# Performance work log

Hardware: AMD Instinct MI355X
Metric: run time of the kernel (lower is better)

## Reference

```python
import jax, jax.numpy as jnp
import numpy as np

N = 20000        # nodes
E = 320000       # edges (avg degree 16)
F_IN = 128       # node_features
F2 = 64          # second_features (per-head out dim, LSTM hidden)
H = 8            # heads
D1 = H * F2      # 512, concat output of GATConv / LSTM input
NEG_SLOPE = 0.2  # GATConv default leaky_relu slope


def _gat_conv(x, src, dst, W, att_src, att_dst, bias):
    """PyG GATConv (concat=True, self-loops added, eval-mode dropout)."""
    n = x.shape[0]
    h = (x @ W).reshape(n, H, -1)                      # [N,H,F]
    a_s = (h * att_src).sum(-1)                        # [N,H]
    a_d = (h * att_dst).sum(-1)                        # [N,H]
    e = jax.nn.leaky_relu(a_s[src] + a_d[dst], NEG_SLOPE)   # [E',H]
    m = jax.ops.segment_max(e, dst, num_segments=n)    # [N,H]
    m = jnp.where(jnp.isfinite(m), m, 0.0)
    ex = jnp.exp(e - m[dst])
    denom = jax.ops.segment_sum(ex, dst, num_segments=n)
    alpha = ex / (denom[dst] + 1e-16)                  # [E',H]
    msg = h[src] * alpha[:, :, None]                   # [E',H,F]
    out = jax.ops.segment_sum(msg, dst, num_segments=n)  # [N,H,F]
    return out.reshape(n, -1) + bias                   # [N,H*F]


def _lstm_step(x, W_ih, W_hh, b_ih, b_hh):
    """Single-timestep PyTorch LSTM with zero initial (h0, c0). x: [N,D1]."""
    h0 = jnp.zeros((x.shape[0], F2), x.dtype)
    gates = x @ W_ih.T + b_ih + h0 @ W_hh.T + b_hh     # [N,4*F2]
    i, f, g, o = jnp.split(gates, 4, axis=-1)
    c = jax.nn.sigmoid(f) * 0.0 + jax.nn.sigmoid(i) * jnp.tanh(g)
    h = jax.nn.sigmoid(o) * jnp.tanh(c)
    return h, (h, c)


def setup_inputs() -> dict:
    key = jax.random.key(0)
    ks = jax.random.split(key, 16)

    def glorot(k, shape, fan_in):
        return jax.random.normal(k, shape, jnp.float32) * (1.0 / np.sqrt(fan_in))

    return {
        "x": jax.random.normal(ks[0], (N, F_IN), jnp.float32),
        "edge_index": jax.random.randint(ks[1], (2, E), 0, N, jnp.int32),
        "edge_weight": jax.random.uniform(ks[2], (E,), jnp.float32),
        # GATConv 1: F_IN -> H*F2
        "W1": glorot(ks[3], (F_IN, H * F2), F_IN),
        "att_src1": glorot(ks[4], (H, F2), F2),
        "att_dst1": glorot(ks[5], (H, F2), F2),
        "bias1": jnp.zeros((H * F2,), jnp.float32),
        # LSTM: input D1 -> hidden F2
        "W_ih": glorot(ks[6], (4 * F2, D1), D1),
        "W_hh": glorot(ks[7], (4 * F2, F2), F2),
        "b_ih": jnp.zeros((4 * F2,), jnp.float32),
        "b_hh": jnp.zeros((4 * F2,), jnp.float32),
        # GATConv 2: F2 -> H*F2
        "W2": glorot(ks[8], (F2, H * F2), F2),
        "att_src2": glorot(ks[9], (H, F2), F2),
        "att_dst2": glorot(ks[10], (H, F2), F2),
        "bias2": jnp.zeros((H * F2,), jnp.float32),
    }


def reference(x, edge_index, edge_weight, W1, att_src1, att_dst1, bias1,
              W_ih, W_hh, b_ih, b_hh, W2, att_src2, att_dst2, bias2):
    # edge_weight is accepted but unused, matching the original forward.
    loops = jnp.arange(N, dtype=edge_index.dtype)
    src = jnp.concatenate([edge_index[0], loops])      # add self-loops (PyG default)
    dst = jnp.concatenate([edge_index[1], loops])

    h = _gat_conv(x, src, dst, W1, att_src1, att_dst1, bias1)   # [N,512]
    h, hidden2 = _lstm_step(h, W_ih, W_hh, b_ih, b_hh)          # [N,64]
    h = jax.nn.relu(h)
    h = _gat_conv(h, src, dst, W2, att_src2, att_dst2, bias2)   # [N,512]
    return jax.nn.softmax(h, axis=1)
```

## Files before the change

### kernel.cpp

```cpp
#include <hip/hip_runtime.h>
#include <math.h>
#include <stdint.h>


__global__ void count_kernel(const int* __restrict__ dst, int* __restrict__ deg, int E) {
  int i = blockIdx.x * 256 + threadIdx.x;
  if (i < E) atomicAdd(&deg[dst[i]], 1);
}

__global__ void scan_kernel(const int* __restrict__ deg, int* __restrict__ rowptr, int n) {
  __shared__ int buf[1024];
  const int tid = threadIdx.x;
  const int i0 = tid * 20;
  int v[20];
  int tsum = 0;
#pragma unroll
  for (int k = 0; k < 20; ++k) {
    int i = i0 + k;
    v[k] = (i < n) ? (deg[i] + 1) : 0;
    tsum += v[k];
  }
  int incl = tsum;
  buf[tid] = incl;
  __syncthreads();
  for (int s = 1; s < 1024; s <<= 1) {
    int t = (tid >= (unsigned)s) ? buf[tid - s] : 0;
    __syncthreads();
    incl += t;
    buf[tid] = incl;
    __syncthreads();
  }
  int excl = incl - tsum;
#pragma unroll
  for (int k = 0; k < 20; ++k) {
    int i = i0 + k;
    if (i < n) rowptr[i] = excl;
    excl += v[k];
  }
  if (tid == 1023) rowptr[n] = incl;
}

__global__ void scatter_kernel(const int* __restrict__ src, const int* __restrict__ dst,
                               const int* __restrict__ rowptr, int* __restrict__ wp,
                               int* __restrict__ col, int E, int n) {
  int i = blockIdx.x * 256 + threadIdx.x;
  if (i < E) {
    int d = dst[i];
    int p = rowptr[d] + atomicAdd(&wp[d], 1);
    col[p] = src[i];
  } else if (i < E + n) {
    int d = i - E;
    int p = rowptr[d] + atomicAdd(&wp[d], 1);
    col[p] = d;
  }
}


__device__ __forceinline__ uint16_t bf16r(float x) {
  uint32_t u = __float_as_uint(x);
  return (uint16_t)((u + 0x7FFFu + ((u >> 16) & 1u)) >> 16);
}
__device__ __forceinline__ void bfsplit(float x, uint16_t& h, uint16_t& l) {
  h = bf16r(x);
  float hf = __uint_as_float((uint32_t)h << 16);
  l = bf16r(x - hf);
}
__device__ __forceinline__ void store4split(uint16_t* oh, uint16_t* ol, float4 v) {
  ushort4 h, l;
  bfsplit(v.x, h.x, l.x); bfsplit(v.y, h.y, l.y);
  bfsplit(v.z, h.z, l.z); bfsplit(v.w, h.w, l.w);
  *reinterpret_cast<ushort4*>(oh) = h;
  *reinterpret_cast<ushort4*>(ol) = l;
}

__device__ __forceinline__ void gload16(const uint16_t* g, uint16_t* l) {
  __builtin_amdgcn_global_load_lds(
      (const __attribute__((address_space(1))) uint32_t*)g,
      (__attribute__((address_space(3))) uint32_t*)l, 16, 0, 0);
}

using bf16x8 = __attribute__((ext_vector_type(8))) short;
using f32x4  = __attribute__((ext_vector_type(4))) float;


template <bool SPLIT_OUT>
__global__ __launch_bounds__(256) void gemm_mfma(
    const uint16_t* __restrict__ Ah, const uint16_t* __restrict__ Al,
    const uint16_t* __restrict__ Bh, const uint16_t* __restrict__ Bl,
    float* __restrict__ C, uint16_t* __restrict__ Ch, uint16_t* __restrict__ Cl,
    const float* __restrict__ bias,
    int M, int K, int lda, int aZ, int bZ, int ldc, int cZ, int biasZ) {
  constexpr int BM = 64, BN = 64, BK = 64;
  constexpr int PL = BM * BK;
  __shared__ __align__(16) uint16_t sAh[2 * PL], sAl[2 * PL];
  __shared__ __align__(16) uint16_t sBh[2 * PL], sBl[2 * PL];
  const int z = blockIdx.z;
  Ah += (size_t)z * aZ; Al += (size_t)z * aZ;
  Bh += (size_t)z * bZ; Bl += (size_t)z * bZ;
  const int tid = threadIdx.x;
  const int wid = tid >> 6, lane = tid & 63;
  int L = blockIdx.x + gridDim.x * blockIdx.y;
  int nwg = gridDim.x * gridDim.y;
  int q = nwg >> 3, r = nwg & 7;
  int xcd = L & 7, gix = L >> 3;
  int base = (xcd < r) ? xcd * (q + 1) : r * (q + 1) + (xcd - r) * q;
  int w = base + gix;
  const int bm = (w / gridDim.x) * BM;
  const int bn = (w % gridDim.x) * BN;
  const int fr = lane & 15;
  const int kg = lane >> 4;
  const int mbase = wid * 16;
  f32x4 acc[4] = {};

  auto stage = [&](int sb, int k0) {
#pragma unroll
    for (int j = 0; j < 2; ++j) {
      int idx = (wid * 2 + j) * 64 + lane;
      int row = idx >> 3, c = idx & 7;
      int rg = min(bm + row, M - 1);
      size_t goA = (size_t)rg * lda + k0 + ((c ^ (row & 7)) << 3);
      uint16_t* ldst = sAh + sb * PL + (wid * 2 + j) * 512;
      gload16(Ah + goA, ldst);
      gload16(Al + goA, sAl + sb * PL + (wid * 2 + j) * 512);
      size_t goB = (size_t)(bn + row) * K + k0 + ((c ^ (row & 7)) << 3);
      gload16(Bh + goB, sBh + sb * PL + (wid * 2 + j) * 512);
      gload16(Bl + goB, sBl + sb * PL + (wid * 2 + j) * 512);
    }
  };

  stage(0, 0);
  __syncthreads();
  int buf = 0;
  for (int k0 = 0; k0 < K; k0 += BK) {
    const bool more = (k0 + BK) < K;
    if (more) stage(buf ^ 1, k0 + BK);
    const char* pAh = (const char*)sAh + buf * (PL * 2);
    const char* pAl = (const char*)sAl + buf * (PL * 2);
    const char* pBh = (const char*)sBh + buf * (PL * 2);
    const char* pBl = (const char*)sBl + buf * (PL * 2);
#pragma unroll
    for (int ks = 0; ks < 2; ++ks) {
      const int kc = ks * 4 + kg;
      bf16x8 ah, al, bh[4], bl[4];
      {
        int m = mbase + fr;
        int off = m * 128 + ((kc ^ (m & 7)) << 4);
        ah = *reinterpret_cast<const bf16x8*>(pAh + off);
        al = *reinterpret_cast<const bf16x8*>(pAl + off);
      }
#pragma unroll
      for (int j = 0; j < 4; ++j) {
        int n = j * 16 + fr;
        int off = n * 128 + ((kc ^ (n & 7)) << 4);
        bh[j] = *reinterpret_cast<const bf16x8*>(pBh + off);
        bl[j] = *reinterpret_cast<const bf16x8*>(pBl + off);
      }
#pragma unroll
      for (int j = 0; j < 4; ++j) {
        acc[j] = __builtin_amdgcn_mfma_f32_16x16x32_bf16(ah, bh[j], acc[j], 0, 0, 0);
        acc[j] = __builtin_amdgcn_mfma_f32_16x16x32_bf16(al, bh[j], acc[j], 0, 0, 0);
        acc[j] = __builtin_amdgcn_mfma_f32_16x16x32_bf16(ah, bl[j], acc[j], 0, 0, 0);
      }
    }
    if (more) {
      __syncthreads();
      buf ^= 1;
    }
  }
  float bz[4];
#pragma unroll
  for (int j = 0; j < 4; ++j)
    bz[j] = bias ? bias[(size_t)z * biasZ + bn + j * 16 + fr] : 0.f;
  if (SPLIT_OUT) {
    Ch += (size_t)z * cZ;
    Cl += (size_t)z * cZ;
  } else {
    C += (size_t)z * cZ;
  }
  {
    int mr = bm + mbase + kg * 4;
#pragma unroll
    for (int rr = 0; rr < 4; ++rr) {
      int m = mr + rr;
      if (m < M) {
#pragma unroll
        for (int j = 0; j < 4; ++j) {
          float v = acc[j][rr] + bz[j];
          size_t o = (size_t)m * ldc + bn + j * 16 + fr;
          if (SPLIT_OUT) {
            uint16_t h, l;
            bfsplit(v, h, l);
            Ch[o] = h; Cl[o] = l;
          } else {
            C[o] = v;
          }
        }
      }
    }
  }
}


__global__ void prep_all_kernel(const float* __restrict__ W_ih, const float* __restrict__ b_ih,
                                const float* __restrict__ b_hh, const float* __restrict__ W1,
                                const float* __restrict__ as1, const float* __restrict__ ad1,
                                const float* __restrict__ W2, const float* __restrict__ as2,
                                const float* __restrict__ ad2,
                                int* __restrict__ degwp,
                                uint16_t* __restrict__ Wtbh, uint16_t* __restrict__ Wtbl,
                                uint16_t* __restrict__ Bt1h, uint16_t* __restrict__ Bt1l,
                                uint16_t* __restrict__ Bt2h, uint16_t* __restrict__ Bt2l,
                                float* __restrict__ bsum, float* __restrict__ watt1,
                                float* __restrict__ watt2, int n2) {
  int idx = blockIdx.x * 256 + threadIdx.x;
  if (idx < n2) {
    degwp[idx] = 0;
    return;
  }
  int t = idx - n2;
  if (t < 98304) {
    int jp = t >> 9, k = t & 511;
    int j = (jp < 64) ? jp : jp + 64;
    uint16_t h, l;
    bfsplit(W_ih[(size_t)j * 512 + k], h, l);
    Wtbh[t] = h; Wtbl[t] = l;
    return;
  }
  t -= 98304;
  if (t < 65536) {
    int n = t >> 7, k = t & 127;
    uint16_t h, l;
    bfsplit(W1[(size_t)k * 512 + n], h, l);
    Bt1h[t] = h; Bt1l[t] = l;
    return;
  }
  t -= 65536;
  if (t < 32768) {
    int n = t >> 6, k = t & 63;
    uint16_t h, l;
    bfsplit(W2[(size_t)k * 512 + n], h, l);
    Bt2h[t] = h; Bt2l[t] = l;
    return;
  }
  t -= 32768;
  if (t < 192) {
    int j = (t < 64) ? t : t + 64;
    bsum[t] = b_ih[j] + b_hh[j];
    return;
  }
  t -= 192;
  if (t < 2048) {
    int f = t >> 4, c = t & 15;
    int k = c & 7;
    const float* att = ((c < 8) ? as1 : ad1) + k * 64;
    const float* w = W1 + (size_t)f * 512 + k * 64;
    float s = 0.f;
#pragma unroll
    for (int j = 0; j < 64; ++j) s = fmaf(w[j], att[j], s);
    watt1[t] = s;
    return;
  }
  t -= 2048;
  if (t < 1024) {
    int f = t >> 4, c = t & 15;
    int k = c & 7;
    const float* att = ((c < 8) ? as2 : ad2) + k * 64;
    const float* w = W2 + (size_t)f * 512 + k * 64;
    float s = 0.f;
#pragma unroll
    for (int j = 0; j < 64; ++j) s = fmaf(w[j], att[j], s);
    watt2[t] = s;
  }
}


template <int F>
__global__ __launch_bounds__(256) void attcoef_kernel(
    const float* __restrict__ feat, const float* __restrict__ watt,
    float* __restrict__ a_s, float* __restrict__ a_d, int n) {
  __shared__ float rows[16 * F];
  __shared__ float wbuf[F * 16];
  const int n0 = blockIdx.x * 16;
  const int tid = threadIdx.x;
  if (n0 + 16 <= n) {
    const float4* g = reinterpret_cast<const float4*>(feat + (size_t)n0 * F);
    float4* l = reinterpret_cast<float4*>(rows);
    for (int i = tid; i < 16 * F / 4; i += 256) l[i] = g[i];
  } else {
    for (int i = tid; i < 16 * F; i += 256) {
      int r = i / F;
      rows[i] = (n0 + r < n) ? feat[(size_t)(n0 + r) * F + (i - r * F)] : 0.f;
    }
  }
  {
    const float4* g = reinterpret_cast<const float4*>(watt);
    float4* l = reinterpret_cast<float4*>(wbuf);
    for (int i = tid; i < F * 16 / 4; i += 256) l[i] = g[i];
  }
  __syncthreads();
  const int local = tid >> 4, c = tid & 15;
  float s = 0.f;
#pragma unroll 8
  for (int f = 0; f < F; ++f) s = fmaf(rows[local * F + f], wbuf[f * 16 + c], s);
  const int node = n0 + local;
  if (node < n) {
    if (c < 8) a_s[(size_t)node * 8 + c] = s;
    else       a_d[(size_t)node * 8 + (c - 8)] = s;
  }
}


template <int F>
__global__ __launch_bounds__(256) void gat_aggregate_wave(
    const float* __restrict__ feat, const float* __restrict__ a_s,
    const float* __restrict__ a_d, const int* __restrict__ rowptr,
    const int* __restrict__ col, uint16_t* __restrict__ aggH,
    uint16_t* __restrict__ aggL, int n) {
  constexpr int FL = F / 4;
  constexpr int HPW = (F == 128) ? 4 : 2;
  __shared__ float s_ex[4][8][8];
  __shared__ int s_cols[4][8];
  const int wid = threadIdx.x >> 6;
  const int lane = threadIdx.x & 63;
  const int node = blockIdx.x * 4 + wid;
  if (node >= n) return;
  const int start = rowptr[node];
  const int deg = rowptr[node + 1] - start;
  const int j = lane >> 3;
  const int h = lane & 7;
  const int f4 = lane & (FL - 1);
  const int hbase = (lane / FL) * HPW;
  const float adh = a_d[(size_t)node * 8 + h];
  float dpart = 0.f;
  float4 acc[HPW];
#pragma unroll
  for (int q = 0; q < HPW; ++q) acc[q] = make_float4(0.f, 0.f, 0.f, 0.f);

  for (int c0 = 0; c0 < deg; c0 += 8) {
    float ex = 0.f;
    int sj = 0;
    if (c0 + j < deg) {
      sj = col[start + c0 + j];
      float v = a_s[(size_t)sj * 8 + h] + adh;
      v = (v > 0.f) ? v : 0.2f * v;
      ex = __expf(v);
    }
    s_ex[wid][j][h] = ex;
    if (h == 0) s_cols[wid][j] = sj;
    dpart += ex;
    __builtin_amdgcn_wave_barrier();
    if (deg - c0 >= 8) {
      float4 fv[8];
#pragma unroll
      for (int e = 0; e < 8; ++e) {
        int s = s_cols[wid][e];
        fv[e] = *reinterpret_cast<const float4*>(feat + (size_t)s * F + f4 * 4);
      }
#pragma unroll
      for (int e = 0; e < 8; ++e) {
        float alv[HPW];
        if constexpr (HPW == 4)
          *reinterpret_cast<float4*>(alv) =
              *reinterpret_cast<const float4*>(&s_ex[wid][e][hbase]);
        else
          *reinterpret_cast<float2*>(alv) =
              *reinterpret_cast<const float2*>(&s_ex[wid][e][hbase]);
#pragma unroll
        for (int q = 0; q < HPW; ++q) {
          acc[q].x = fmaf(alv[q], fv[e].x, acc[q].x);
          acc[q].y = fmaf(alv[q], fv[e].y, acc[q].y);
          acc[q].z = fmaf(alv[q], fv[e].z, acc[q].z);
          acc[q].w = fmaf(alv[q], fv[e].w, acc[q].w);
        }
      }
    } else {
      const int ce = deg - c0;
      for (int e = 0; e < ce; ++e) {
        int s = s_cols[wid][e];
        float4 fv = *reinterpret_cast<const float4*>(feat + (size_t)s * F + f4 * 4);
        float alv[HPW];
        if constexpr (HPW == 4)
          *reinterpret_cast<float4*>(alv) =
              *reinterpret_cast<const float4*>(&s_ex[wid][e][hbase]);
        else
          *reinterpret_cast<float2*>(alv) =
              *reinterpret_cast<const float2*>(&s_ex[wid][e][hbase]);
#pragma unroll
        for (int q = 0; q < HPW; ++q) {
          acc[q].x = fmaf(alv[q], fv.x, acc[q].x);
          acc[q].y = fmaf(alv[q], fv.y, acc[q].y);
          acc[q].z = fmaf(alv[q], fv.z, acc[q].z);
          acc[q].w = fmaf(alv[q], fv.w, acc[q].w);
        }
      }
    }
    __builtin_amdgcn_wave_barrier();
  }
  dpart += __shfl_xor(dpart, 8);
  dpart += __shfl_xor(dpart, 16);
  dpart += __shfl_xor(dpart, 32);
#pragma unroll
  for (int q = 0; q < HPW; ++q) {
    float dq = __shfl(dpart, hbase + q);
    float dinv = 1.f / (dq + 1e-16f);
    size_t off = (size_t)node * 8 * F + (size_t)(hbase + q) * F + f4 * 4;
    float4 o = make_float4(acc[q].x * dinv, acc[q].y * dinv,
                           acc[q].z * dinv, acc[q].w * dinv);
    store4split(aggH + off, aggL + off, o);
  }
}


__global__ __launch_bounds__(256) void lstm_act_attcoef_kernel(
    const float* __restrict__ gates, const float* __restrict__ bsum,
    const float* __restrict__ watt2, float* __restrict__ h2,
    float* __restrict__ a_s2, float* __restrict__ a_d2, int n) {
  __shared__ float h2t[4][64];
  __shared__ float wbuf[64 * 16];
  const int tid = threadIdx.x;
  reinterpret_cast<float4*>(wbuf)[tid] = reinterpret_cast<const float4*>(watt2)[tid];
  const int nl = tid >> 6, j = tid & 63;
  const int node = blockIdx.x * 4 + nl;
  float hv = 0.f;
  if (node < n) {
    const float* g0 = gates + (size_t)node * 192;
    float iv = g0[j] + bsum[j];
    float gv = g0[64 + j] + bsum[64 + j];
    float ov = g0[128 + j] + bsum[128 + j];
    float c = (1.f / (1.f + __expf(-iv))) * tanhf(gv);
    hv = fmaxf((1.f / (1.f + __expf(-ov))) * tanhf(c), 0.f);
    h2[(size_t)node * 64 + j] = hv;
  }
  h2t[nl][j] = hv;
  __syncthreads();
  if (j < 16 && node < n) {
    float s = 0.f;
#pragma unroll 16
    for (int f = 0; f < 64; ++f) s = fmaf(h2t[nl][f], wbuf[f * 16 + j], s);
    if (j < 8) a_s2[(size_t)node * 8 + j] = s;
    else       a_d2[(size_t)node * 8 + (j - 8)] = s;
  }
}


__global__ __launch_bounds__(256) void softmax512_wave(const float* __restrict__ in,
                                                       float* __restrict__ out, int n) {
  const int wid = threadIdx.x >> 6, lane = threadIdx.x & 63;
  const int node = blockIdx.x * 4 + wid;
  if (node >= n) return;
  const float4* ip = reinterpret_cast<const float4*>(in + (size_t)node * 512);
  float4 v0 = ip[lane];
  float4 v1 = ip[64 + lane];
  float m = fmaxf(fmaxf(fmaxf(v0.x, v0.y), fmaxf(v0.z, v0.w)),
                  fmaxf(fmaxf(v1.x, v1.y), fmaxf(v1.z, v1.w)));
#pragma unroll
  for (int d = 1; d < 64; d <<= 1) m = fmaxf(m, __shfl_xor(m, d));
  float4 e0, e1;
  e0.x = __expf(v0.x - m); e0.y = __expf(v0.y - m);
  e0.z = __expf(v0.z - m); e0.w = __expf(v0.w - m);
  e1.x = __expf(v1.x - m); e1.y = __expf(v1.y - m);
  e1.z = __expf(v1.z - m); e1.w = __expf(v1.w - m);
  float s = e0.x + e0.y + e0.z + e0.w + e1.x + e1.y + e1.z + e1.w;
#pragma unroll
  for (int d = 1; d < 64; d <<= 1) s += __shfl_xor(s, d);
  float inv = 1.f / s;
  e0.x *= inv; e0.y *= inv; e0.z *= inv; e0.w *= inv;
  e1.x *= inv; e1.y *= inv; e1.z *= inv; e1.w *= inv;
  float4* op = reinterpret_cast<float4*>(out + (size_t)node * 512);
  op[lane] = e0;
  op[64 + lane] = e1;
}


extern "C" void kernel_launch(void* const* d_in, const int* in_sizes, int n_in,
                              void* d_out, int out_size, void* d_ws, size_t ws_size,
                              hipStream_t stream) {
  const float* x      = (const float*)d_in[0];
  const int*   ei     = (const int*)d_in[1];
  const float* W1     = (const float*)d_in[3];
  const float* att_s1 = (const float*)d_in[4];
  const float* att_d1 = (const float*)d_in[5];
  const float* bias1  = (const float*)d_in[6];
  const float* W_ih   = (const float*)d_in[7];
  const float* b_ih   = (const float*)d_in[9];
  const float* b_hh   = (const float*)d_in[10];
  const float* W2     = (const float*)d_in[11];
  const float* att_s2 = (const float*)d_in[12];
  const float* att_d2 = (const float*)d_in[13];
  const float* bias2  = (const float*)d_in[14];
  float* out = (float*)d_out;

  const int N = in_sizes[0] / 128;
  const int E = in_sizes[1] / 2;
  const int* src = ei;
  const int* dst = ei + E;

  char* p = (char*)d_ws;
  auto alloc = [&](size_t bytes) {
    char* r = p;
    p += (bytes + 255) & ~(size_t)255;
    return r;
  };
  char* slotA = alloc((size_t)N * 4096);
  char* slotB = alloc((size_t)N * 2048);
  float* a_s1 = (float*)alloc((size_t)N * 8 * 4);
  float* a_d1 = (float*)alloc((size_t)N * 8 * 4);
  float* a_s2 = (float*)alloc((size_t)N * 8 * 4);
  float* a_d2 = (float*)alloc((size_t)N * 8 * 4);
  float* watt1 = (float*)alloc(128 * 16 * 4);
  float* watt2 = (float*)alloc(64 * 16 * 4);
  uint16_t* Wtbh = (uint16_t*)alloc((size_t)192 * 512 * 2);
  uint16_t* Wtbl = (uint16_t*)alloc((size_t)192 * 512 * 2);
  uint16_t* Bt1h = (uint16_t*)alloc((size_t)512 * 128 * 2);
  uint16_t* Bt1l = (uint16_t*)alloc((size_t)512 * 128 * 2);
  uint16_t* Bt2h = (uint16_t*)alloc((size_t)512 * 64 * 2);
  uint16_t* Bt2l = (uint16_t*)alloc((size_t)512 * 64 * 2);
  float* bsum = (float*)alloc(192 * 4);
  int* deg    = (int*)alloc((size_t)2 * N * 4);
  int* wp     = deg + N;
  int* rowptr = (int*)alloc((size_t)(N + 1) * 4);
  int* col    = (int*)alloc((size_t)(E + N) * 4);

  uint16_t* agg1h = (uint16_t*)slotA;
  uint16_t* agg1l = agg1h + (size_t)N * 1024;
  float* gates2 = (float*)slotA;
  float* h2 = (float*)(slotA + (size_t)N * 768);
  uint16_t* agg2h = (uint16_t*)(slotA + (size_t)N * 1024);
  uint16_t* agg2l = agg2h + (size_t)N * 512;
  uint16_t* g1h = (uint16_t*)slotB;
  uint16_t* g1l = g1h + (size_t)N * 512;
  float* h3p = (float*)slotB;

  {
    int total = 2 * N + 98304 + 65536 + 32768 + 192 + 2048 + 1024;
    prep_all_kernel<<<(total + 255) / 256, 256, 0, stream>>>(
        W_ih, b_ih, b_hh, W1, att_s1, att_d1, W2, att_s2, att_d2,
        deg, Wtbh, Wtbl, Bt1h, Bt1l, Bt2h, Bt2l, bsum, watt1, watt2, 2 * N);
  }

  count_kernel<<<(E + 255) / 256, 256, 0, stream>>>(dst, deg, E);
  scan_kernel<<<1, 1024, 0, stream>>>(deg, rowptr, N);
  scatter_kernel<<<(E + N + 255) / 256, 256, 0, stream>>>(src, dst, rowptr, wp, col, E, N);

  const int NYB = (N + 63) / 64;

  attcoef_kernel<128><<<(N + 15) / 16, 256, 0, stream>>>(x, watt1, a_s1, a_d1, N);
  gat_aggregate_wave<128><<<(N + 3) / 4, 256, 0, stream>>>(x, a_s1, a_d1, rowptr, col,
                                                           agg1h, agg1l, N);
  {
    dim3 g(1, NYB, 8);
    gemm_mfma<true><<<g, 256, 0, stream>>>(
        agg1h, agg1l, Bt1h, Bt1l, nullptr, g1h, g1l, bias1,
        N, 128, 1024, 128, 64 * 128, 512, 64, 64);
  }

  {
    dim3 g(3, NYB, 1);
    gemm_mfma<false><<<g, 256, 0, stream>>>(
        g1h, g1l, Wtbh, Wtbl, gates2, nullptr, nullptr, nullptr,
        N, 512, 512, 0, 0, 192, 0, 0);
  }
  lstm_act_attcoef_kernel<<<(N + 3) / 4, 256, 0, stream>>>(gates2, bsum, watt2,
                                                           h2, a_s2, a_d2, N);

  gat_aggregate_wave<64><<<(N + 3) / 4, 256, 0, stream>>>(h2, a_s2, a_d2, rowptr, col,
                                                          agg2h, agg2l, N);
  {
    dim3 g(1, NYB, 8);
    gemm_mfma<false><<<g, 256, 0, stream>>>(
        agg2h, agg2l, Bt2h, Bt2l, h3p, nullptr, nullptr, bias2,
        N, 64, 512, 64, 64 * 64, 512, 64, 64);
  }
  softmax512_wave<<<(N + 3) / 4, 256, 0, stream>>>(h3p, out, N);
}
```

Measured before the change: 321.0 us.

## Fuse GAT neighbor aggregation with per-head projection GEMM via LDS tiles

```diff
diff --git a/kernel.cpp b/kernel.cpp
--- a/kernel.cpp
+++ b/kernel.cpp
@@ -64,13 +64,6 @@
   h = bf16r(x);
   float hf = __uint_as_float((uint32_t)h << 16);
   l = bf16r(x - hf);
-}
-__device__ __forceinline__ void store4split(uint16_t* oh, uint16_t* ol, float4 v) {
-  ushort4 h, l;
-  bfsplit(v.x, h.x, l.x); bfsplit(v.y, h.y, l.y);
-  bfsplit(v.z, h.z, l.z); bfsplit(v.w, h.w, l.w);
-  *reinterpret_cast<ushort4*>(oh) = h;
-  *reinterpret_cast<ushort4*>(ol) = l;
 }
 
 __device__ __forceinline__ void gload16(const uint16_t* g, uint16_t* l) {
@@ -119,8 +112,7 @@
       int row = idx >> 3, c = idx & 7;
       int rg = min(bm + row, M - 1);
       size_t goA = (size_t)rg * lda + k0 + ((c ^ (row & 7)) << 3);
-      uint16_t* ldst = sAh + sb * PL + (wid * 2 + j) * 512;
-      gload16(Ah + goA, ldst);
+      gload16(Ah + goA, sAh + sb * PL + (wid * 2 + j) * 512);
       gload16(Al + goA, sAl + sb * PL + (wid * 2 + j) * 512);
       size_t goB = (size_t)(bn + row) * K + k0 + ((c ^ (row & 7)) << 3);
       gload16(Bh + goB, sBh + sb * PL + (wid * 2 + j) * 512);
@@ -310,103 +302,152 @@
 }
 
 
-template <int F>
-__global__ __launch_bounds__(256) void gat_aggregate_wave(
+template <int F, bool SPLIT_OUT>
+__global__ __launch_bounds__(512) void gat_fused(
     const float* __restrict__ feat, const float* __restrict__ a_s,
     const float* __restrict__ a_d, const int* __restrict__ rowptr,
-    const int* __restrict__ col, uint16_t* __restrict__ aggH,
-    uint16_t* __restrict__ aggL, int n) {
+    const int* __restrict__ col,
+    const uint16_t* __restrict__ Bh, const uint16_t* __restrict__ Bl,
+    const float* __restrict__ bias, float* __restrict__ C,
+    uint16_t* __restrict__ Ch, uint16_t* __restrict__ Cl, int n) {
   constexpr int FL = F / 4;
-  constexpr int HPW = (F == 128) ? 4 : 2;
-  __shared__ float s_ex[4][8][8];
-  __shared__ int s_cols[4][8];
-  const int wid = threadIdx.x >> 6;
-  const int lane = threadIdx.x & 63;
-  const int node = blockIdx.x * 4 + wid;
-  if (node >= n) return;
-  const int start = rowptr[node];
-  const int deg = rowptr[node + 1] - start;
-  const int j = lane >> 3;
-  const int h = lane & 7;
-  const int f4 = lane & (FL - 1);
-  const int hbase = (lane / FL) * HPW;
-  const float adh = a_d[(size_t)node * 8 + h];
-  float dpart = 0.f;
-  float4 acc[HPW];
-#pragma unroll
-  for (int q = 0; q < HPW; ++q) acc[q] = make_float4(0.f, 0.f, 0.f, 0.f);
-
-  for (int c0 = 0; c0 < deg; c0 += 8) {
-    float ex = 0.f;
-    int sj = 0;
-    if (c0 + j < deg) {
-      sj = col[start + c0 + j];
-      float v = a_s[(size_t)sj * 8 + h] + adh;
-      v = (v > 0.f) ? v : 0.2f * v;
-      ex = __expf(v);
-    }
-    s_ex[wid][j][h] = ex;
-    if (h == 0) s_cols[wid][j] = sj;
-    dpart += ex;
-    __builtin_amdgcn_wave_barrier();
-    if (deg - c0 >= 8) {
-      float4 fv[8];
-#pragma unroll
-      for (int e = 0; e < 8; ++e) {
-        int s = s_cols[wid][e];
-        fv[e] = *reinterpret_cast<const float4*>(feat + (size_t)s * F + f4 * 4);
-      }
-#pragma unroll
-      for (int e = 0; e < 8; ++e) {
-        float alv[HPW];
-        if constexpr (HPW == 4)
-          *reinterpret_cast<float4*>(alv) =
-              *reinterpret_cast<const float4*>(&s_ex[wid][e][hbase]);
-        else
-          *reinterpret_cast<float2*>(alv) =
-              *reinterpret_cast<const float2*>(&s_ex[wid][e][hbase]);
-#pragma unroll
-        for (int q = 0; q < HPW; ++q) {
-          acc[q].x = fmaf(alv[q], fv[e].x, acc[q].x);
-          acc[q].y = fmaf(alv[q], fv[e].y, acc[q].y);
-          acc[q].z = fmaf(alv[q], fv[e].z, acc[q].z);
-          acc[q].w = fmaf(alv[q], fv[e].w, acc[q].w);
+  constexpr int HPW = FL / 8;
+  __shared__ uint16_t AtH[8][16][F];
+  __shared__ uint16_t AtL[8][16][F];
+  const int tid = threadIdx.x;
+  const int wid = tid >> 6, lane = tid & 63;
+  const int nb0 = blockIdx.x * 16;
+  const int j = lane >> 3, h = lane & 7;
+  const int grp = lane / FL, f4 = lane & (FL - 1);
+  const int hbase = grp * HPW;
+
+  for (int i = 0; i < 2; ++i) {
+    const int r = wid * 2 + i;
+    const int node = nb0 + r;
+    int start = 0, deg = 0;
+    float adh = 0.f;
+    if (node < n) {
+      start = rowptr[node];
+      deg = rowptr[node + 1] - start;
+      adh = a_d[(size_t)node * 8 + h];
+    }
+    float dpart = 0.f;
+    float4 acc[HPW];
+#pragma unroll
+    for (int q = 0; q < HPW; ++q) acc[q] = make_float4(0.f, 0.f, 0.f, 0.f);
+
+    for (int c0 = 0; c0 < deg; c0 += 8) {
+      float ex = 0.f;
+      int sj = 0;
+      if (c0 + j < deg) {
+        sj = col[start + c0 + j];
+        float v = a_s[(size_t)sj * 8 + h] + adh;
+        v = (v > 0.f) ? v : 0.2f * v;
+        ex = __expf(v);
+      }
+      dpart += ex;
+      if (deg - c0 >= 8) {
+        int se[8];
+        float4 fv[8];
+#pragma unroll
+        for (int e = 0; e < 8; ++e) se[e] = __shfl(sj, e * 8);
+#pragma unroll
+        for (int e = 0; e < 8; ++e)
+          fv[e] = *reinterpret_cast<const float4*>(feat + (size_t)se[e] * F + f4 * 4);
+#pragma unroll
+        for (int e = 0; e < 8; ++e) {
+          float alv[HPW];
+#pragma unroll
+          for (int q = 0; q < HPW; ++q) alv[q] = __shfl(ex, e * 8 + hbase + q);
+#pragma unroll
+          for (int q = 0; q < HPW; ++q) {
+            acc[q].x = fmaf(alv[q], fv[e].x, acc[q].x);
+            acc[q].y = fmaf(alv[q], fv[e].y, acc[q].y);
+            acc[q].z = fmaf(alv[q], fv[e].z, acc[q].z);
+            acc[q].w = fmaf(alv[q], fv[e].w, acc[q].w);
+          }
         }
-      }
-    } else {
-      const int ce = deg - c0;
-      for (int e = 0; e < ce; ++e) {
-        int s = s_cols[wid][e];
-        float4 fv = *reinterpret_cast<const float4*>(feat + (size_t)s * F + f4 * 4);
-        float alv[HPW];
-        if constexpr (HPW == 4)
-          *reinterpret_cast<float4*>(alv) =
-              *reinterpret_cast<const float4*>(&s_ex[wid][e][hbase]);
-        else
-          *reinterpret_cast<float2*>(alv) =
-              *reinterpret_cast<const float2*>(&s_ex[wid][e][hbase]);
-#pragma unroll
-        for (int q = 0; q < HPW; ++q) {
-          acc[q].x = fmaf(alv[q], fv.x, acc[q].x);
-          acc[q].y = fmaf(alv[q], fv.y, acc[q].y);
-          acc[q].z = fmaf(alv[q], fv.z, acc[q].z);
-          acc[q].w = fmaf(alv[q], fv.w, acc[q].w);
+      } else {
+        const int ce = deg - c0;
+        for (int e = 0; e < ce; ++e) {
+          int s = __shfl(sj, e * 8);
+          float4 fv = *reinterpret_cast<const float4*>(feat + (size_t)s * F + f4 * 4);
+          float alv[HPW];
+#pragma unroll
+          for (int q = 0; q < HPW; ++q) alv[q] = __shfl(ex, e * 8 + hbase + q);
+#pragma unroll
+          for (int q = 0; q < HPW; ++q) {
+            acc[q].x = fmaf(alv[q], fv.x, acc[q].x);
+            acc[q].y = fmaf(alv[q], fv.y, acc[q].y);
+            acc[q].z = fmaf(alv[q], fv.z, acc[q].z);
+            acc[q].w = fmaf(alv[q], fv.w, acc[q].w);
+          }
         }
       }
     }
-    __builtin_amdgcn_wave_barrier();
-  }
-  dpart += __shfl_xor(dpart, 8);
-  dpart += __shfl_xor(dpart, 16);
-  dpart += __shfl_xor(dpart, 32);
-#pragma unroll
-  for (int q = 0; q < HPW; ++q) {
-    float dq = __shfl(dpart, hbase + q);
-    float dinv = 1.f / (dq + 1e-16f);
-    size_t off = (size_t)node * 8 * F + (size_t)(hbase + q) * F + f4 * 4;
-    float4 o = make_float4(acc[q].x * dinv, acc[q].y * dinv,
-                           acc[q].z * dinv, acc[q].w * dinv);
-    store4split(aggH + off, aggL + off, o);
+    dpart += __shfl_xor(dpart, 8);
+    dpart += __shfl_xor(dpart, 16);
+    dpart += __shfl_xor(dpart, 32);
+    const int swz = (f4 * 8) ^ ((r & 7) << 4);
+#pragma unroll
+    for (int q = 0; q < HPW; ++q) {
+      float dq = __shfl(dpart, hbase + q);
+      float dinv = 1.f / (dq + 1e-16f);
+      ushort4 hi4, lo4;
+      bfsplit(acc[q].x * dinv, hi4.x, lo4.x);
+      bfsplit(acc[q].y * dinv, hi4.y, lo4.y);
+      bfsplit(acc[q].z * dinv, hi4.z, lo4.z);
+      bfsplit(acc[q].w * dinv, hi4.w, lo4.w);
+      *reinterpret_cast<ushort4*>(
+          reinterpret_cast<char*>(&AtH[hbase + q][r][0]) + swz) = hi4;
+      *reinterpret_cast<ushort4*>(
+          reinterpret_cast<char*>(&AtL[hbase + q][r][0]) + swz) = lo4;
+    }
+  }
+  __syncthreads();
+
+  const int hd = wid;
+  const int fr = lane & 15, kg = lane >> 4;
+  const uint16_t* Bhh = Bh + (size_t)(hd * 64) * F;
+  const uint16_t* Blh = Bl + (size_t)(hd * 64) * F;
+  f32x4 pacc[4] = {};
+#pragma unroll
+  for (int ks = 0; ks < F / 32; ++ks) {
+    const int kc = ks * 4 + kg;
+    const int aoff = (kc * 16) ^ ((fr & 7) << 4);
+    bf16x8 ah = *reinterpret_cast<const bf16x8*>(
+        reinterpret_cast<const char*>(&AtH[hd][fr][0]) + aoff);
+    bf16x8 al = *reinterpret_cast<const bf16x8*>(
+        reinterpret_cast<const char*>(&AtL[hd][fr][0]) + aoff);
+#pragma unroll
+    for (int jf = 0; jf < 4; ++jf) {
+      const size_t bro = (size_t)(jf * 16 + fr) * F + kc * 8;
+      bf16x8 bh = *reinterpret_cast<const bf16x8*>(Bhh + bro);
+      bf16x8 bl = *reinterpret_cast<const bf16x8*>(Blh + bro);
+      pacc[jf] = __builtin_amdgcn_mfma_f32_16x16x32_bf16(ah, bh, pacc[jf], 0, 0, 0);
+      pacc[jf] = __builtin_amdgcn_mfma_f32_16x16x32_bf16(al, bh, pacc[jf], 0, 0, 0);
+      pacc[jf] = __builtin_amdgcn_mfma_f32_16x16x32_bf16(ah, bl, pacc[jf], 0, 0, 0);
+    }
+  }
+#pragma unroll
+  for (int jf = 0; jf < 4; ++jf) {
+    const int colg = hd * 64 + jf * 16 + fr;
+    const float bz = bias[colg];
+#pragma unroll
+    for (int rr = 0; rr < 4; ++rr) {
+      int m = nb0 + kg * 4 + rr;
+      if (m < n) {
+        float v = pacc[jf][rr] + bz;
+        size_t o = (size_t)m * 512 + colg;
+        if (SPLIT_OUT) {
+          uint16_t hh2, ll2;
+          bfsplit(v, hh2, ll2);
+          Ch[o] = hh2; Cl[o] = ll2;
+        } else {
+          C[o] = v;
+        }
+      }
+    }
   }
 }
 
@@ -521,12 +562,8 @@
   int* rowptr = (int*)alloc((size_t)(N + 1) * 4);
   int* col    = (int*)alloc((size_t)(E + N) * 4);
 
-  uint16_t* agg1h = (uint16_t*)slotA;
-  uint16_t* agg1l = agg1h + (size_t)N * 1024;
   float* gates2 = (float*)slotA;
   float* h2 = (float*)(slotA + (size_t)N * 768);
-  uint16_t* agg2h = (uint16_t*)(slotA + (size_t)N * 1024);
-  uint16_t* agg2l = agg2h + (size_t)N * 512;
   uint16_t* g1h = (uint16_t*)slotB;
   uint16_t* g1l = g1h + (size_t)N * 512;
   float* h3p = (float*)slotB;
@@ -542,20 +579,12 @@
   scan_kernel<<<1, 1024, 0, stream>>>(deg, rowptr, N);
   scatter_kernel<<<(E + N + 255) / 256, 256, 0, stream>>>(src, dst, rowptr, wp, col, E, N);
 
-  const int NYB = (N + 63) / 64;
-
   attcoef_kernel<128><<<(N + 15) / 16, 256, 0, stream>>>(x, watt1, a_s1, a_d1, N);
-  gat_aggregate_wave<128><<<(N + 3) / 4, 256, 0, stream>>>(x, a_s1, a_d1, rowptr, col,
-                                                           agg1h, agg1l, N);
+  gat_fused<128, true><<<(N + 15) / 16, 512, 0, stream>>>(
+      x, a_s1, a_d1, rowptr, col, Bt1h, Bt1l, bias1, nullptr, g1h, g1l, N);
+
   {
-    dim3 g(1, NYB, 8);
-    gemm_mfma<true><<<g, 256, 0, stream>>>(
-        agg1h, agg1l, Bt1h, Bt1l, nullptr, g1h, g1l, bias1,
-        N, 128, 1024, 128, 64 * 128, 512, 64, 64);
-  }
-
-  {
-    dim3 g(3, NYB, 1);
+    dim3 g(3, (N + 63) / 64, 1);
     gemm_mfma<false><<<g, 256, 0, stream>>>(
         g1h, g1l, Wtbh, Wtbl, gates2, nullptr, nullptr, nullptr,
         N, 512, 512, 0, 0, 192, 0, 0);
@@ -563,13 +592,7 @@
   lstm_act_attcoef_kernel<<<(N + 3) / 4, 256, 0, stream>>>(gates2, bsum, watt2,
                                                            h2, a_s2, a_d2, N);
 
-  gat_aggregate_wave<64><<<(N + 3) / 4, 256, 0, stream>>>(h2, a_s2, a_d2, rowptr, col,
-                                                          agg2h, agg2l, N);
-  {
-    dim3 g(1, NYB, 8);
-    gemm_mfma<false><<<g, 256, 0, stream>>>(
-        agg2h, agg2l, Bt2h, Bt2l, h3p, nullptr, nullptr, bias2,
-        N, 64, 512, 64, 64 * 64, 512, 64, 64);
-  }
+  gat_fused<64, false><<<(N + 15) / 16, 512, 0, stream>>>(
+      h2, a_s2, a_d2, rowptr, col, Bt2h, Bt2l, bias2, h3p, nullptr, nullptr, N);
   softmax512_wave<<<(N + 3) / 4, 256, 0, stream>>>(h3p, out, N);
 }
```

After: 377.0 us. 1.17x slower.
